# Optimization experiments

Measured on AMD Instinct MI355X. Metric: run time of the kernel, lower is better.

Reference implementation:

```python
import jax, jax.numpy as jnp
import numpy as np

EPS = 1e-3  # tfa LayerNormLSTMCell default norm epsilon

def _ln(z, g, b):
    # layernorm over last axis, per gate: z [B,4,U], g/b [4,U]
    mu = jnp.mean(z, axis=-1, keepdims=True)
    var = jnp.mean((z - mu) ** 2, axis=-1, keepdims=True)
    return g * (z - mu) * jax.lax.rsqrt(var + EPS) + b

def setup_inputs() -> dict:
    key = jax.random.key(0)
    ks = jax.random.split(key, 12)
    B, T, D, U, C = 1024, 100, 300, 512, 14
    sc = lambda k, shape, fan: jax.random.normal(k, shape, jnp.float32) * (1.0 / np.sqrt(fan))
    return {
        "x": jax.random.normal(ks[0], (B, T, D), jnp.float32),
        "mask": jax.random.randint(ks[1], (B, T), 0, 2).astype(jnp.int32),
        # layer 0 (input dim D)
        "W0": sc(ks[2], (D, 4 * U), D), "U0": sc(ks[3], (U, 4 * U), U),
        "b0": jnp.zeros((4 * U,), jnp.float32),
        "g0": jnp.ones((4, U), jnp.float32), "be0": jnp.zeros((4, U), jnp.float32),
        # layer 1 (input dim U)
        "W1": sc(ks[4], (U, 4 * U), U), "U1": sc(ks[5], (U, 4 * U), U),
        "b1": jnp.zeros((4 * U,), jnp.float32),
        "g1": jnp.ones((4, U), jnp.float32), "be1": jnp.zeros((4, U), jnp.float32),
        # dense softmax head
        "Wd": sc(ks[6], (U, C), U), "bd": jnp.zeros((C,), jnp.float32),
    }

def reference(x, mask, W0, U0, b0, g0, be0, W1, U1, b1, g1, be1, Wd, bd):
    B, T, D = x.shape
    U = W0.shape[1] // 4
    params = [(W0, U0, b0, g0, be0), (W1, U1, b1, g1, be1)]

    def step(carry, tins):
        hs, cs = carry
        xt, mt = tins                      # xt [B,D_in], mt [B]
        m = (mt > 0)[:, None]
        inp = xt
        new_hs, new_cs = [], []
        for l in range(2):
            W, Uw, b, g, be = params[l]
            z = (inp @ W + hs[l] @ Uw).reshape(B, 4, U)
            z = _ln(z, g, be) + b.reshape(4, U)
            i_g = jax.nn.sigmoid(z[:, 0])
            f_g = jax.nn.sigmoid(z[:, 1])
            c_g = jnp.tanh(z[:, 2])
            o_g = jax.nn.sigmoid(z[:, 3])
            c = f_g * cs[l] + i_g * c_g
            h = o_g * jnp.tanh(c)
            # keras RNN masking: carry state through masked steps
            h = jnp.where(m, h, hs[l])
            c = jnp.where(m, c, cs[l])
            new_hs.append(h); new_cs.append(c)
            inp = h
        return (tuple(new_hs), tuple(new_cs)), None

    z0 = jnp.zeros((B, U), x.dtype)
    carry0 = ((z0, z0), (z0, z0))
    xs = (jnp.swapaxes(x, 0, 1), mask.T)   # time-major [T,B,...]
    (hs, _), _ = jax.lax.scan(step, carry0, xs)
    h_top = hs[-1]                          # [B,U] = last valid output via mask carry
    return jax.nn.softmax(h_top @ Wd + bd, axis=-1)
```

## Files before the change

### kernel.cpp

```cpp
#include <hip/hip_runtime.h>


typedef _Float16 f16;
typedef _Float16 f16x8 __attribute__((ext_vector_type(8)));
typedef float f32x4 __attribute__((ext_vector_type(4)));

__global__ __launch_bounds__(256) void transpose_f16(
    const float* __restrict__ W, f16* __restrict__ Bt, int K, int N, int Kp,
    int k_off) {
  __shared__ float s[32][33];
  int n0 = blockIdx.x * 32, k0 = blockIdx.y * 32;
  int tid = threadIdx.x, c = tid & 31, r8 = tid >> 5;
  for (int rr = r8; rr < 32; rr += 8) {
    int k = k0 + rr;
    s[rr][c] = (k < K) ? W[(long)k * N + (n0 + c)] : 0.0f;
  }
  __syncthreads();
  for (int rr = r8; rr < 32; rr += 8)
    Bt[(long)(n0 + rr) * Kp + k_off + (k0 + c)] = (f16)s[c][rr];
}

#define MFMAS(AF, BF)                                                                   \
  acc[0][0] = __builtin_amdgcn_mfma_f32_16x16x32_f16(AF[0], BF[0], acc[0][0], 0, 0, 0); \
  acc[0][1] = __builtin_amdgcn_mfma_f32_16x16x32_f16(AF[0], BF[1], acc[0][1], 0, 0, 0); \
  acc[1][0] = __builtin_amdgcn_mfma_f32_16x16x32_f16(AF[1], BF[0], acc[1][0], 0, 0, 0); \
  acc[1][1] = __builtin_amdgcn_mfma_f32_16x16x32_f16(AF[1], BF[1], acc[1][1], 0, 0, 0); \
  acc[2][0] = __builtin_amdgcn_mfma_f32_16x16x32_f16(AF[2], BF[0], acc[2][0], 0, 0, 0); \
  acc[2][1] = __builtin_amdgcn_mfma_f32_16x16x32_f16(AF[2], BF[1], acc[2][1], 0, 0, 0); \
  acc[3][0] = __builtin_amdgcn_mfma_f32_16x16x32_f16(AF[3], BF[0], acc[3][0], 0, 0, 0); \
  acc[3][1] = __builtin_amdgcn_mfma_f32_16x16x32_f16(AF[3], BF[1], acc[3][1], 0, 0, 0);

#define LOADAB(AF, BF, A0, B0, LDB, K0)                    \
  AF[0] = *(const f16x8*)((A0) + (K0));                    \
  AF[1] = *(const f16x8*)((A0) + 16 * 1024 + (K0));        \
  AF[2] = *(const f16x8*)((A0) + 32 * 1024 + (K0));        \
  AF[3] = *(const f16x8*)((A0) + 48 * 1024 + (K0));        \
  BF[0] = *(const f16x8*)((B0) + (K0));                    \
  BF[1] = *(const f16x8*)((B0) + 16 * (LDB) + (K0));

#define GEMM_PIPE4(A0, B0, LDB, KTOT)                            \
  {                                                              \
    f16x8 aA[4], bA[2], aB[4], bB[2];                            \
    f16x8 aC[4], bC[2], aD[4], bD[2];                            \
    LOADAB(aA, bA, A0, B0, LDB, 0)                               \
    LOADAB(aB, bB, A0, B0, LDB, 32)                              \
    LOADAB(aC, bC, A0, B0, LDB, 64)                              \
    LOADAB(aD, bD, A0, B0, LDB, 96)                              \
    for (int k0 = 0; k0 + 224 < (KTOT); k0 += 128) {             \
      MFMAS(aA, bA) LOADAB(aA, bA, A0, B0, LDB, k0 + 128)        \
      MFMAS(aB, bB) LOADAB(aB, bB, A0, B0, LDB, k0 + 160)        \
      MFMAS(aC, bC) LOADAB(aC, bC, A0, B0, LDB, k0 + 192)       \
      MFMAS(aD, bD) LOADAB(aD, bD, A0, B0, LDB, k0 + 224)        \
    }                                                            \
    MFMAS(aA, bA) MFMAS(aB, bB) MFMAS(aC, bC) MFMAS(aD, bD)      \
  }

#define LOADX(AF, BF, K0)                                            \
  {                                                                  \
    _Pragma("unroll") for (int i = 0; i < 4; ++i) {                  \
      f32x4 lo = *(const f32x4*)(ax + (long)i * 4800 + (K0));        \
      f32x4 hi = *(const f32x4*)(ax + (long)i * 4800 + (K0) + 4);    \
      _Pragma("unroll") for (int e = 0; e < 4; ++e) {                \
        AF[i][e] = (f16)lo[e];                                       \
        AF[i][4 + e] = (f16)hi[e];                                   \
      }                                                              \
    }                                                                \
    BF[0] = *(const f16x8*)(bw + (K0));                              \
    BF[1] = *(const f16x8*)(bw + 16 * 320 + (K0));                   \
  }

__global__ __launch_bounds__(256) void gemm_x0(
    const float* __restrict__ x, const f16* __restrict__ W0t,
    f16* __restrict__ z0x) {
  __shared__ f16 st[64][136];
  int tid = threadIdx.x;
  int lane = tid & 63, w = tid >> 6;
  int l15 = lane & 15, quad = lane >> 4;
  long bn0 = (long)blockIdx.x * 128 + w * 32;
  long bm0 = (long)blockIdx.y * 64;
  const float* ax = x + (bm0 + l15) * 300L + quad * 8;
  const f16* bw = W0t + (bn0 + l15) * 320L + quad * 8;

  f32x4 acc[4][2] = {};
  f16x8 af0[4], bf0[2], af1[4], bf1[2];
  LOADX(af0, bf0, 0)
  for (int k0 = 0; k0 < 224; k0 += 64) {
    LOADX(af1, bf1, k0 + 32)
    MFMAS(af0, bf0)
    LOADX(af0, bf0, k0 + 64)
    MFMAS(af1, bf1)
  }
  {
#pragma unroll
    for (int i = 0; i < 4; ++i) {
      long rb = (bm0 + l15 + i * 16) * 300L;
#pragma unroll
      for (int e = 0; e < 8; ++e) {
        int k = 288 + quad * 8 + e;
        af1[i][e] = (k < 300) ? (f16)x[rb + k] : (f16)0.f;
      }
    }
    bf1[0] = *(const f16x8*)(bw + 288);
    bf1[1] = *(const f16x8*)(bw + 16 * 320 + 288);
  }
  MFMAS(af0, bf0)
  MFMAS(af1, bf1)

#pragma unroll
  for (int i = 0; i < 4; ++i)
#pragma unroll
    for (int j = 0; j < 2; ++j)
#pragma unroll
      for (int r = 0; r < 4; ++r)
        st[i * 16 + quad * 4 + r][w * 32 + j * 16 + l15] = (f16)acc[i][j][r];
  __syncthreads();

  {
    int r = tid >> 2, cc = (tid & 3) * 32;
    unsigned rr = (unsigned)(bm0 + r);
    unsigned b = rr / 100u, t = rr - b * 100u;
    f16* dst = z0x + (long)t * 2097152 + (long)b * 2048 + (long)blockIdx.x * 128 + cc;
    const f16x8* s8 = (const f16x8*)&st[r][cc];
    f16x8* d8 = (f16x8*)dst;
    d8[0] = s8[0]; d8[1] = s8[1]; d8[2] = s8[2]; d8[3] = s8[3];
  }
}

__global__ __launch_bounds__(256, 2) void gemm_step(
    const float* __restrict__ xt, const f16* __restrict__ h01,
    const f16* __restrict__ W0t, const f16* __restrict__ U0t,
    const f16* __restrict__ WU1t, const f16* __restrict__ cin0,
    float* __restrict__ zA, float* __restrict__ zB, int do0, int do1) {
  int prob = blockIdx.y >> 4;
  if (prob ? !do1 : !do0) return;
  int tid = threadIdx.x;
  int lane = tid & 63, w = tid >> 6;
  int l15 = lane & 15, quad = lane >> 4;
  long bn0 = (long)blockIdx.x * 128 + w * 32;
  long bm0 = (long)(blockIdx.y & 15) * 64;
  long arow = (bm0 + l15) * 1024 + quad * 8;

  f32x4 acc[4][2] = {};

  if (prob == 0) {
    if (!cin0) {
      const float* ax = xt + (bm0 + l15) * 30000L + quad * 8;
      const f16* bw = W0t + (bn0 + l15) * 320L + quad * 8;
#pragma unroll
      for (int k0 = 0; k0 < 288; k0 += 32) {
        f16x8 af[4], bf[2];
#pragma unroll
        for (int i = 0; i < 4; ++i) {
          f32x4 lo = *(const f32x4*)(ax + (long)i * 480000 + k0);
          f32x4 hi = *(const f32x4*)(ax + (long)i * 480000 + k0 + 4);
#pragma unroll
          for (int e = 0; e < 4; ++e) {
            af[i][e] = (f16)lo[e];
            af[i][4 + e] = (f16)hi[e];
          }
        }
        bf[0] = *(const f16x8*)(bw + k0);
        bf[1] = *(const f16x8*)(bw + 16 * 320 + k0);
        MFMAS(af, bf)
      }
      {
        f16x8 af[4], bf[2];
#pragma unroll
        for (int i = 0; i < 4; ++i) {
          long rb = (bm0 + l15 + i * 16) * 30000L;
#pragma unroll
          for (int e = 0; e < 8; ++e) {
            int k = 288 + quad * 8 + e;
            af[i][e] = (k < 300) ? (f16)xt[rb + k] : (f16)0.f;
          }
        }
        bf[0] = *(const f16x8*)(bw + 288);
        bf[1] = *(const f16x8*)(bw + 16 * 320 + 288);
        MFMAS(af, bf)
      }
    }
    {
      const f16* a0 = h01 + arow;
      const f16* b0 = U0t + (bn0 + l15) * 512L + quad * 8;
      GEMM_PIPE4(a0, b0, 512, 512)
    }
  } else {
    const f16* a0 = h01 + arow;
    const f16* b0 = WU1t + (bn0 + l15) * 1024L + quad * 8;
    GEMM_PIPE4(a0, b0, 1024, 1024)
  }

  float* Z = prob ? zB : zA;
#pragma unroll
  for (int i = 0; i < 4; ++i) {
    long row = bm0 + i * 16 + quad * 4;
#pragma unroll
    for (int j = 0; j < 2; ++j) {
      long col = bn0 + j * 16 + l15;
#pragma unroll
      for (int r = 0; r < 4; ++r) {
        float v = acc[i][j][r];
        if (prob == 0 && cin0) v += (float)cin0[(row + r) * 2048 + col];
        Z[(row + r) * 2048 + col] = v;
      }
    }
  }
}

__global__ __launch_bounds__(256) void ln_gates2(
    const float* __restrict__ zA, const float* __restrict__ zB,
    const float* __restrict__ g0, const float* __restrict__ be0,
    const float* __restrict__ b0, const float* __restrict__ g1,
    const float* __restrict__ be1, const float* __restrict__ b1,
    const int* __restrict__ mask, int t,
    f16* __restrict__ h01, float* __restrict__ c0, float* __restrict__ c1,
    int do0, int do1) {
  __shared__ float act[2048];
  int layer = blockIdx.x >> 10;
  if (layer ? !do1 : !do0) return;
  int b = blockIdx.x & 1023;
  const float* z = layer ? zB : zA;
  const float* gamma = layer ? g1 : g0;
  const float* beta = layer ? be1 : be0;
  const float* bias = layer ? b1 : b0;
  f16* h = h01 + layer * 512;
  float* c = layer ? c1 : c0;
  int tm = layer ? (t - 1) : t;

  int tid = threadIdx.x;
  int w = tid >> 6, lane = tid & 63;

  const float* zb = z + (long)b * 2048 + w * 512;
  f32x4 zv[2];
  float sum = 0.0f, sq = 0.0f;
#pragma unroll
  for (int i = 0; i < 2; ++i) {
    f32x4 v = *(const f32x4*)(zb + lane * 4 + 256 * i);
    zv[i] = v;
#pragma unroll
    for (int e = 0; e < 4; ++e) {
      sum += v[e];
      sq += v[e] * v[e];
    }
  }
#pragma unroll
  for (int off = 32; off; off >>= 1) {
    sum += __shfl_xor(sum, off);
    sq += __shfl_xor(sq, off);
  }
  float mu = sum * (1.0f / 512.0f);
  float var = sq * (1.0f / 512.0f) - mu * mu;
  float is = rsqrtf(var + 1e-3f);

#pragma unroll
  for (int i = 0; i < 2; ++i) {
    int k = w * 512 + lane * 4 + 256 * i;
    f32x4 g = *(const f32x4*)(gamma + k);
    f32x4 be = *(const f32x4*)(beta + k);
    f32x4 bi = *(const f32x4*)(bias + k);
    f32x4 av;
#pragma unroll
    for (int e = 0; e < 4; ++e) {
      float val = g[e] * (zv[i][e] - mu) * is + be[e] + bi[e];
      float a;
      if (w == 2) {
        a = 2.0f / (1.0f + __expf(-2.0f * val)) - 1.0f;
      } else {
        a = 1.0f / (1.0f + __expf(-val));
      }
      av[e] = a;
    }
    *(f32x4*)(act + k) = av;
  }
  __syncthreads();

  bool m = mask[(long)b * 100 + tm] > 0;
#pragma unroll
  for (int i = 0; i < 2; ++i) {
    int u = tid + 256 * i;
    float co = c[(long)b * 512 + u];
    float ho = (float)h[(long)b * 1024 + u];
    float cn = act[512 + u] * co + act[u] * act[1024 + u];
    float th = 2.0f / (1.0f + __expf(-2.0f * cn)) - 1.0f;
    float hn = act[1536 + u] * th;
    h[(long)b * 1024 + u] = (f16)(m ? hn : ho);
    c[(long)b * 512 + u] = m ? cn : co;
  }
}

__global__ __launch_bounds__(64) void head_kernel(
    const f16* __restrict__ h01, const float* __restrict__ Wd,
    const float* __restrict__ bd, float* __restrict__ out) {
  __shared__ float hs[512];
  __shared__ float lg[16];
  int b = blockIdx.x, tid = threadIdx.x;
#pragma unroll
  for (int i = 0; i < 8; ++i)
    hs[tid + 64 * i] = (float)h01[(long)b * 1024 + 512 + tid + 64 * i];
  __syncthreads();
  if (tid < 14) {
    float s = bd[tid];
    for (int k = 0; k < 512; ++k) s += hs[k] * Wd[k * 14 + tid];
    lg[tid] = s;
  }
  __syncthreads();
  if (tid < 14) {
    float mx = lg[0];
#pragma unroll
    for (int i = 1; i < 14; ++i) mx = fmaxf(mx, lg[i]);
    float e = __expf(lg[tid] - mx);
    float den = 0.0f;
#pragma unroll
    for (int i = 0; i < 14; ++i) den += __expf(lg[i] - mx);
    out[(long)b * 14 + tid] = e / den;
  }
}

extern "C" void kernel_launch(void* const* d_in, const int* in_sizes, int n_in,
                              void* d_out, int out_size, void* d_ws, size_t ws_size,
                              hipStream_t stream) {
  const float* x   = (const float*)d_in[0];
  const int* mask  = (const int*)d_in[1];
  const float* W0  = (const float*)d_in[2];
  const float* U0w = (const float*)d_in[3];
  const float* b0  = (const float*)d_in[4];
  const float* g0  = (const float*)d_in[5];
  const float* be0 = (const float*)d_in[6];
  const float* W1  = (const float*)d_in[7];
  const float* U1w = (const float*)d_in[8];
  const float* b1  = (const float*)d_in[9];
  const float* g1  = (const float*)d_in[10];
  const float* be1 = (const float*)d_in[11];
  const float* Wd  = (const float*)d_in[12];
  const float* bd  = (const float*)d_in[13];
  float* out = (float*)d_out;

  char* p = (char*)d_ws;
  const size_t MB = (size_t)1 << 20;
  f16*   h01  = (f16*)(p + 0);
  float* c0   = (float*)(p + 2 * MB);
  float* c1   = (float*)(p + 4 * MB);
  float* zA   = (float*)(p + 6 * MB);
  float* zB   = (float*)(p + 14 * MB);
  f16*   W0t  = (f16*)(p + 22 * MB);
  f16*   U0t  = (f16*)(p + 22 * MB + 1310720);
  f16*   WU1t = (f16*)(p + 22 * MB + 1310720 + 2097152);
  f16*   z0x  = (f16*)(p + 32 * MB);

  const bool hoist = ws_size >= (size_t)432 * MB;

  hipMemsetAsync(p, 0, 6 * MB, stream);

  transpose_f16<<<dim3(64, 10), 256, 0, stream>>>(W0,  W0t, 300, 2048, 320, 0);
  transpose_f16<<<dim3(64, 16), 256, 0, stream>>>(U0w, U0t, 512, 2048, 512, 0);
  transpose_f16<<<dim3(64, 16), 256, 0, stream>>>(W1,  WU1t, 512, 2048, 1024, 0);
  transpose_f16<<<dim3(64, 16), 256, 0, stream>>>(U1w, WU1t, 512, 2048, 1024, 512);

  if (hoist) {
    gemm_x0<<<dim3(16, 1600), 256, 0, stream>>>(x, W0t, z0x);
  }

  for (int t = 0; t <= 100; ++t) {
    int do0 = (t < 100) ? 1 : 0;
    int do1 = (t >= 1) ? 1 : 0;
    const f16* cin0 = hoist ? (z0x + (long)t * 2097152) : nullptr;
    gemm_step<<<dim3(16, 32), 256, 0, stream>>>(
        x + (long)t * 300, h01, W0t, U0t, WU1t, cin0, zA, zB, do0, do1);
    ln_gates2<<<2048, 256, 0, stream>>>(
        zA, zB, g0, be0, b0, g1, be1, b1, mask, t, h01, c0, c1, do0, do1);
  }

  head_kernel<<<1024, 64, 0, stream>>>(h01, Wd, bd, out);
}
```

Before: 5.923 ms.

## Store gate pre-activations in fp16 and stage x tile once in LDS for hoisted GEMM

```diff
diff --git a/kernel.cpp b/kernel.cpp
--- a/kernel.cpp
+++ b/kernel.cpp
@@ -3,6 +3,7 @@
 
 typedef _Float16 f16;
 typedef _Float16 f16x8 __attribute__((ext_vector_type(8)));
+typedef _Float16 f16x4 __attribute__((ext_vector_type(4)));
 typedef float f32x4 __attribute__((ext_vector_type(4)));
 
 __global__ __launch_bounds__(256) void transpose_f16(
@@ -55,74 +56,62 @@
     MFMAS(aA, bA) MFMAS(aB, bB) MFMAS(aC, bC) MFMAS(aD, bD)      \
   }
 
-#define LOADX(AF, BF, K0)                                            \
-  {                                                                  \
-    _Pragma("unroll") for (int i = 0; i < 4; ++i) {                  \
-      f32x4 lo = *(const f32x4*)(ax + (long)i * 4800 + (K0));        \
-      f32x4 hi = *(const f32x4*)(ax + (long)i * 4800 + (K0) + 4);    \
-      _Pragma("unroll") for (int e = 0; e < 4; ++e) {                \
-        AF[i][e] = (f16)lo[e];                                       \
-        AF[i][4 + e] = (f16)hi[e];                                   \
-      }                                                              \
-    }                                                                \
-    BF[0] = *(const f16x8*)(bw + (K0));                              \
-    BF[1] = *(const f16x8*)(bw + 16 * 320 + (K0));                   \
-  }
-
 __global__ __launch_bounds__(256) void gemm_x0(
     const float* __restrict__ x, const f16* __restrict__ W0t,
     f16* __restrict__ z0x) {
+  __shared__ f16 xs[64][328];
   __shared__ f16 st[64][136];
   int tid = threadIdx.x;
+  long bm0 = (long)blockIdx.x * 64;
+
+  for (int p = 0; p < 20; ++p) {
+    unsigned idx = (unsigned)tid + p * 256u;
+    unsigned r = idx / 80u, s = idx - r * 80u;
+    f16x4 h4 = {};
+    if (s < 75u) {
+      f32x4 v = *(const f32x4*)(x + (bm0 + r) * 300L + s * 4u);
+      h4[0] = (f16)v[0]; h4[1] = (f16)v[1];
+      h4[2] = (f16)v[2]; h4[3] = (f16)v[3];
+    }
+    *(f16x4*)&xs[r][s * 4u] = h4;
+  }
+  __syncthreads();
+
   int lane = tid & 63, w = tid >> 6;
   int l15 = lane & 15, quad = lane >> 4;
-  long bn0 = (long)blockIdx.x * 128 + w * 32;
-  long bm0 = (long)blockIdx.y * 64;
-  const float* ax = x + (bm0 + l15) * 300L + quad * 8;
-  const f16* bw = W0t + (bn0 + l15) * 320L + quad * 8;
-
-  f32x4 acc[4][2] = {};
-  f16x8 af0[4], bf0[2], af1[4], bf1[2];
-  LOADX(af0, bf0, 0)
-  for (int k0 = 0; k0 < 224; k0 += 64) {
-    LOADX(af1, bf1, k0 + 32)
-    MFMAS(af0, bf0)
-    LOADX(af0, bf0, k0 + 64)
-    MFMAS(af1, bf1)
-  }
-  {
-#pragma unroll
-    for (int i = 0; i < 4; ++i) {
-      long rb = (bm0 + l15 + i * 16) * 300L;
-#pragma unroll
-      for (int e = 0; e < 8; ++e) {
-        int k = 288 + quad * 8 + e;
-        af1[i][e] = (k < 300) ? (f16)x[rb + k] : (f16)0.f;
-      }
-    }
-    bf1[0] = *(const f16x8*)(bw + 288);
-    bf1[1] = *(const f16x8*)(bw + 16 * 320 + 288);
-  }
-  MFMAS(af0, bf0)
-  MFMAS(af1, bf1)
-
-#pragma unroll
-  for (int i = 0; i < 4; ++i)
-#pragma unroll
-    for (int j = 0; j < 2; ++j)
-#pragma unroll
-      for (int r = 0; r < 4; ++r)
-        st[i * 16 + quad * 4 + r][w * 32 + j * 16 + l15] = (f16)acc[i][j][r];
-  __syncthreads();
-
-  {
-    int r = tid >> 2, cc = (tid & 3) * 32;
-    unsigned rr = (unsigned)(bm0 + r);
-    unsigned b = rr / 100u, t = rr - b * 100u;
-    f16* dst = z0x + (long)t * 2097152 + (long)b * 2048 + (long)blockIdx.x * 128 + cc;
-    const f16x8* s8 = (const f16x8*)&st[r][cc];
-    f16x8* d8 = (f16x8*)dst;
-    d8[0] = s8[0]; d8[1] = s8[1]; d8[2] = s8[2]; d8[3] = s8[3];
+
+  for (int nc = 0; nc < 16; ++nc) {
+    long bn0 = (long)nc * 128 + w * 32;
+    const f16* bw = W0t + (bn0 + l15) * 320L + quad * 8;
+    f32x4 acc[4][2] = {};
+#pragma unroll
+    for (int k0 = 0; k0 < 320; k0 += 32) {
+      f16x8 af[4], bf[2];
+#pragma unroll
+      for (int i = 0; i < 4; ++i)
+        af[i] = *(const f16x8*)&xs[l15 + i * 16][quad * 8 + k0];
+      bf[0] = *(const f16x8*)(bw + k0);
+      bf[1] = *(const f16x8*)(bw + 16 * 320 + k0);
+      MFMAS(af, bf)
+    }
+    __syncthreads();
+#pragma unroll
+    for (int i = 0; i < 4; ++i)
+#pragma unroll
+      for (int j = 0; j < 2; ++j)
+#pragma unroll
+        for (int r = 0; r < 4; ++r)
+          st[i * 16 + quad * 4 + r][w * 32 + j * 16 + l15] = (f16)acc[i][j][r];
+    __syncthreads();
+    {
+      int r = tid >> 2, cc = (tid & 3) * 32;
+      unsigned rr = (unsigned)(bm0 + r);
+      unsigned b = rr / 100u, t = rr - b * 100u;
+      f16* dst = z0x + (long)t * 2097152 + (long)b * 2048 + nc * 128 + cc;
+      const f16x8* s8 = (const f16x8*)&st[r][cc];
+      f16x8* d8 = (f16x8*)dst;
+      d8[0] = s8[0]; d8[1] = s8[1]; d8[2] = s8[2]; d8[3] = s8[3];
+    }
   }
 }
 
@@ -130,7 +119,8 @@
     const float* __restrict__ xt, const f16* __restrict__ h01,
     const f16* __restrict__ W0t, const f16* __restrict__ U0t,
     const f16* __restrict__ WU1t, const f16* __restrict__ cin0,
-    float* __restrict__ zA, float* __restrict__ zB, int do0, int do1) {
+    f16* __restrict__ zA, f16* __restrict__ zB, int do0, int do1) {
+  __shared__ f16 st[64][136];
   int prob = blockIdx.y >> 4;
   if (prob ? !do1 : !do0) return;
   int tid = threadIdx.x;
@@ -190,25 +180,35 @@
     GEMM_PIPE4(a0, b0, 1024, 1024)
   }
 
-  float* Z = prob ? zB : zA;
 #pragma unroll
   for (int i = 0; i < 4; ++i) {
-    long row = bm0 + i * 16 + quad * 4;
 #pragma unroll
     for (int j = 0; j < 2; ++j) {
-      long col = bn0 + j * 16 + l15;
 #pragma unroll
       for (int r = 0; r < 4; ++r) {
         float v = acc[i][j][r];
-        if (prob == 0 && cin0) v += (float)cin0[(row + r) * 2048 + col];
-        Z[(row + r) * 2048 + col] = v;
+        if (prob == 0 && cin0) {
+          long row = bm0 + i * 16 + quad * 4 + r;
+          long col = bn0 + j * 16 + l15;
+          v += (float)cin0[row * 2048 + col];
+        }
+        st[i * 16 + quad * 4 + r][w * 32 + j * 16 + l15] = (f16)v;
       }
     }
   }
+  __syncthreads();
+  {
+    f16* Z = prob ? zB : zA;
+    int r = tid >> 2, cc = (tid & 3) * 32;
+    f16* dst = Z + (bm0 + r) * 2048 + (long)blockIdx.x * 128 + cc;
+    const f16x8* s8 = (const f16x8*)&st[r][cc];
+    f16x8* d8 = (f16x8*)dst;
+    d8[0] = s8[0]; d8[1] = s8[1]; d8[2] = s8[2]; d8[3] = s8[3];
+  }
 }
 
 __global__ __launch_bounds__(256) void ln_gates2(
-    const float* __restrict__ zA, const float* __restrict__ zB,
+    const f16* __restrict__ zA, const f16* __restrict__ zB,
     const float* __restrict__ g0, const float* __restrict__ be0,
     const float* __restrict__ b0, const float* __restrict__ g1,
     const float* __restrict__ be1, const float* __restrict__ b1,
@@ -219,7 +219,7 @@
   int layer = blockIdx.x >> 10;
   if (layer ? !do1 : !do0) return;
   int b = blockIdx.x & 1023;
-  const float* z = layer ? zB : zA;
+  const f16* z = layer ? zB : zA;
   const float* gamma = layer ? g1 : g0;
   const float* beta = layer ? be1 : be0;
   const float* bias = layer ? b1 : b0;
@@ -230,18 +230,15 @@
   int tid = threadIdx.x;
   int w = tid >> 6, lane = tid & 63;
 
-  const float* zb = z + (long)b * 2048 + w * 512;
-  f32x4 zv[2];
+  f16x8 v8 = *(const f16x8*)(z + (long)b * 2048 + w * 512 + lane * 8);
+  float zv[8];
   float sum = 0.0f, sq = 0.0f;
 #pragma unroll
-  for (int i = 0; i < 2; ++i) {
-    f32x4 v = *(const f32x4*)(zb + lane * 4 + 256 * i);
-    zv[i] = v;
-#pragma unroll
-    for (int e = 0; e < 4; ++e) {
-      sum += v[e];
-      sq += v[e] * v[e];
-    }
+  for (int e = 0; e < 8; ++e) {
+    float v = (float)v8[e];
+    zv[e] = v;
+    sum += v;
+    sq += v * v;
   }
 #pragma unroll
   for (int off = 32; off; off >>= 1) {
@@ -252,16 +249,16 @@
   float var = sq * (1.0f / 512.0f) - mu * mu;
   float is = rsqrtf(var + 1e-3f);
 
+  int k = w * 512 + lane * 8;
 #pragma unroll
   for (int i = 0; i < 2; ++i) {
-    int k = w * 512 + lane * 4 + 256 * i;
-    f32x4 g = *(const f32x4*)(gamma + k);
-    f32x4 be = *(const f32x4*)(beta + k);
-    f32x4 bi = *(const f32x4*)(bias + k);
+    f32x4 g = *(const f32x4*)(gamma + k + 4 * i);
+    f32x4 be = *(const f32x4*)(beta + k + 4 * i);
+    f32x4 bi = *(const f32x4*)(bias + k + 4 * i);
     f32x4 av;
 #pragma unroll
     for (int e = 0; e < 4; ++e) {
-      float val = g[e] * (zv[i][e] - mu) * is + be[e] + bi[e];
+      float val = g[e] * (zv[4 * i + e] - mu) * is + be[e] + bi[e];
       float a;
       if (w == 2) {
         a = 2.0f / (1.0f + __expf(-2.0f * val)) - 1.0f;
@@ -270,7 +267,7 @@
       }
       av[e] = a;
     }
-    *(f32x4*)(act + k) = av;
+    *(f32x4*)(act + k + 4 * i) = av;
   }
   __syncthreads();
 
@@ -340,11 +337,11 @@
   f16*   h01  = (f16*)(p + 0);
   float* c0   = (float*)(p + 2 * MB);
   float* c1   = (float*)(p + 4 * MB);
-  float* zA   = (float*)(p + 6 * MB);
-  float* zB   = (float*)(p + 14 * MB);
-  f16*   W0t  = (f16*)(p + 22 * MB);
-  f16*   U0t  = (f16*)(p + 22 * MB + 1310720);
-  f16*   WU1t = (f16*)(p + 22 * MB + 1310720 + 2097152);
+  f16*   zA   = (f16*)(p + 6 * MB);
+  f16*   zB   = (f16*)(p + 10 * MB);
+  f16*   W0t  = (f16*)(p + 14 * MB);
+  f16*   U0t  = (f16*)(p + 14 * MB + 1310720);
+  f16*   WU1t = (f16*)(p + 14 * MB + 1310720 + 2097152);
   f16*   z0x  = (f16*)(p + 32 * MB);
 
   const bool hoist = ws_size >= (size_t)432 * MB;
@@ -357,7 +354,7 @@
   transpose_f16<<<dim3(64, 16), 256, 0, stream>>>(U1w, WU1t, 512, 2048, 1024, 512);
 
   if (hoist) {
-    gemm_x0<<<dim3(16, 1600), 256, 0, stream>>>(x, W0t, z0x);
+    gemm_x0<<<1600, 256, 0, stream>>>(x, W0t, z0x);
   }
 
   for (int t = 0; t <= 100; ++t) {
```

Result: no change. 6.006 ms (+1.4%).

## Enlarge per-step GEMM tiles and stage input tile in LDS for x-projection

Applied to the files above, without the earlier changes.

```diff
diff --git a/kernel.cpp b/kernel.cpp
--- a/kernel.cpp
+++ b/kernel.cpp
@@ -3,6 +3,7 @@
 
 typedef _Float16 f16;
 typedef _Float16 f16x8 __attribute__((ext_vector_type(8)));
+typedef _Float16 f16x4 __attribute__((ext_vector_type(4)));
 typedef float f32x4 __attribute__((ext_vector_type(4)));
 
 __global__ __launch_bounds__(256) void transpose_f16(
@@ -30,164 +31,130 @@
   acc[3][0] = __builtin_amdgcn_mfma_f32_16x16x32_f16(AF[3], BF[0], acc[3][0], 0, 0, 0); \
   acc[3][1] = __builtin_amdgcn_mfma_f32_16x16x32_f16(AF[3], BF[1], acc[3][1], 0, 0, 0);
 
-#define LOADAB(AF, BF, A0, B0, LDB, K0)                    \
+__global__ __launch_bounds__(256) void gemm_x0(
+    const float* __restrict__ x, long lda, const f16* __restrict__ W0t,
+    f16* __restrict__ z0x, int full) {
+  __shared__ f16 xs[64][340];
+  __shared__ f16 st[64][136];
+  int tid = threadIdx.x;
+  long bm0 = (long)blockIdx.x * 64;
+
+  for (int p = 0; p < 20; ++p) {
+    unsigned idx = (unsigned)tid + p * 256u;
+    unsigned r = idx / 80u, s = idx - r * 80u;
+    f16x4 h4 = {};
+    if (s < 75u) {
+      f32x4 v = *(const f32x4*)(x + (bm0 + r) * lda + s * 4u);
+      h4[0] = (f16)v[0]; h4[1] = (f16)v[1];
+      h4[2] = (f16)v[2]; h4[3] = (f16)v[3];
+    }
+    *(f16x4*)&xs[r][s * 4u] = h4;
+  }
+  __syncthreads();
+
+  int lane = tid & 63, w = tid >> 6;
+  int l15 = lane & 15, quad = lane >> 4;
+
+  for (int nc = 0; nc < 16; ++nc) {
+    long bn0 = (long)nc * 128 + w * 32;
+    const f16* bw = W0t + (bn0 + l15) * 320L + quad * 8;
+    f32x4 acc[4][2] = {};
+#pragma unroll
+    for (int k0 = 0; k0 < 320; k0 += 32) {
+      f16x8 af[4], bf[2];
+#pragma unroll
+      for (int i = 0; i < 4; ++i)
+        af[i] = *(const f16x8*)&xs[l15 + i * 16][quad * 8 + k0];
+      bf[0] = *(const f16x8*)(bw + k0);
+      bf[1] = *(const f16x8*)(bw + 16 * 320 + k0);
+      MFMAS(af, bf)
+    }
+    __syncthreads();
+#pragma unroll
+    for (int i = 0; i < 4; ++i)
+#pragma unroll
+      for (int j = 0; j < 2; ++j)
+#pragma unroll
+        for (int r = 0; r < 4; ++r)
+          st[i * 16 + quad * 4 + r][w * 32 + j * 16 + l15] = (f16)acc[i][j][r];
+    __syncthreads();
+    {
+      int r = tid >> 2, cc = (tid & 3) * 32;
+      f16* dst;
+      if (full) {
+        unsigned rr = (unsigned)(bm0 + r);
+        unsigned b = rr / 100u, t = rr - b * 100u;
+        dst = z0x + (long)t * 2097152 + (long)b * 2048 + nc * 128 + cc;
+      } else {
+        dst = z0x + (bm0 + r) * 2048 + nc * 128 + cc;
+      }
+      const f16x8* s8 = (const f16x8*)&st[r][cc];
+      f16x8* d8 = (f16x8*)dst;
+      d8[0] = s8[0]; d8[1] = s8[1]; d8[2] = s8[2]; d8[3] = s8[3];
+    }
+  }
+}
+
+#define LD8(AF, BF, A0, B0, LDB, K0)                       \
   AF[0] = *(const f16x8*)((A0) + (K0));                    \
   AF[1] = *(const f16x8*)((A0) + 16 * 1024 + (K0));        \
   AF[2] = *(const f16x8*)((A0) + 32 * 1024 + (K0));        \
   AF[3] = *(const f16x8*)((A0) + 48 * 1024 + (K0));        \
   BF[0] = *(const f16x8*)((B0) + (K0));                    \
-  BF[1] = *(const f16x8*)((B0) + 16 * (LDB) + (K0));
-
-#define GEMM_PIPE4(A0, B0, LDB, KTOT)                            \
+  BF[1] = *(const f16x8*)((B0) + 16 * (LDB) + (K0));       \
+  BF[2] = *(const f16x8*)((B0) + 32 * (LDB) + (K0));       \
+  BF[3] = *(const f16x8*)((B0) + 48 * (LDB) + (K0));
+
+#define MM16(AF, BF)                                                              \
+  {                                                                               \
+    _Pragma("unroll") for (int i_ = 0; i_ < 4; ++i_)                              \
+    _Pragma("unroll") for (int j_ = 0; j_ < 4; ++j_)                              \
+      acc[i_][j_] = __builtin_amdgcn_mfma_f32_16x16x32_f16(AF[i_], BF[j_],        \
+                                                            acc[i_][j_], 0, 0, 0); \
+  }
+
+#define GEMM_PIPE4W(A0, B0, LDB, KTOT)                           \
   {                                                              \
-    f16x8 aA[4], bA[2], aB[4], bB[2];                            \
-    f16x8 aC[4], bC[2], aD[4], bD[2];                            \
-    LOADAB(aA, bA, A0, B0, LDB, 0)                               \
-    LOADAB(aB, bB, A0, B0, LDB, 32)                              \
-    LOADAB(aC, bC, A0, B0, LDB, 64)                              \
-    LOADAB(aD, bD, A0, B0, LDB, 96)                              \
+    f16x8 aA[4], bA[4], aB[4], bB[4];                            \
+    f16x8 aC[4], bC[4], aD[4], bD[4];                            \
+    LD8(aA, bA, A0, B0, LDB, 0)                                  \
+    LD8(aB, bB, A0, B0, LDB, 32)                                 \
+    LD8(aC, bC, A0, B0, LDB, 64)                                 \
+    LD8(aD, bD, A0, B0, LDB, 96)                                 \
     for (int k0 = 0; k0 + 224 < (KTOT); k0 += 128) {             \
-      MFMAS(aA, bA) LOADAB(aA, bA, A0, B0, LDB, k0 + 128)        \
-      MFMAS(aB, bB) LOADAB(aB, bB, A0, B0, LDB, k0 + 160)        \
-      MFMAS(aC, bC) LOADAB(aC, bC, A0, B0, LDB, k0 + 192)       \
-      MFMAS(aD, bD) LOADAB(aD, bD, A0, B0, LDB, k0 + 224)        \
+      MM16(aA, bA) LD8(aA, bA, A0, B0, LDB, k0 + 128)            \
+      MM16(aB, bB) LD8(aB, bB, A0, B0, LDB, k0 + 160)            \
+      MM16(aC, bC) LD8(aC, bC, A0, B0, LDB, k0 + 192)            \
+      MM16(aD, bD) LD8(aD, bD, A0, B0, LDB, k0 + 224)            \
     }                                                            \
-    MFMAS(aA, bA) MFMAS(aB, bB) MFMAS(aC, bC) MFMAS(aD, bD)      \
-  }
-
-#define LOADX(AF, BF, K0)                                            \
-  {                                                                  \
-    _Pragma("unroll") for (int i = 0; i < 4; ++i) {                  \
-      f32x4 lo = *(const f32x4*)(ax + (long)i * 4800 + (K0));        \
-      f32x4 hi = *(const f32x4*)(ax + (long)i * 4800 + (K0) + 4);    \
-      _Pragma("unroll") for (int e = 0; e < 4; ++e) {                \
-        AF[i][e] = (f16)lo[e];                                       \
-        AF[i][4 + e] = (f16)hi[e];                                   \
-      }                                                              \
-    }                                                                \
-    BF[0] = *(const f16x8*)(bw + (K0));                              \
-    BF[1] = *(const f16x8*)(bw + 16 * 320 + (K0));                   \
-  }
-
-__global__ __launch_bounds__(256) void gemm_x0(
-    const float* __restrict__ x, const f16* __restrict__ W0t,
-    f16* __restrict__ z0x) {
-  __shared__ f16 st[64][136];
-  int tid = threadIdx.x;
-  int lane = tid & 63, w = tid >> 6;
-  int l15 = lane & 15, quad = lane >> 4;
-  long bn0 = (long)blockIdx.x * 128 + w * 32;
-  long bm0 = (long)blockIdx.y * 64;
-  const float* ax = x + (bm0 + l15) * 300L + quad * 8;
-  const f16* bw = W0t + (bn0 + l15) * 320L + quad * 8;
-
-  f32x4 acc[4][2] = {};
-  f16x8 af0[4], bf0[2], af1[4], bf1[2];
-  LOADX(af0, bf0, 0)
-  for (int k0 = 0; k0 < 224; k0 += 64) {
-    LOADX(af1, bf1, k0 + 32)
-    MFMAS(af0, bf0)
-    LOADX(af0, bf0, k0 + 64)
-    MFMAS(af1, bf1)
-  }
-  {
-#pragma unroll
-    for (int i = 0; i < 4; ++i) {
-      long rb = (bm0 + l15 + i * 16) * 300L;
-#pragma unroll
-      for (int e = 0; e < 8; ++e) {
-        int k = 288 + quad * 8 + e;
-        af1[i][e] = (k < 300) ? (f16)x[rb + k] : (f16)0.f;
-      }
-    }
-    bf1[0] = *(const f16x8*)(bw + 288);
-    bf1[1] = *(const f16x8*)(bw + 16 * 320 + 288);
-  }
-  MFMAS(af0, bf0)
-  MFMAS(af1, bf1)
-
-#pragma unroll
-  for (int i = 0; i < 4; ++i)
-#pragma unroll
-    for (int j = 0; j < 2; ++j)
-#pragma unroll
-      for (int r = 0; r < 4; ++r)
-        st[i * 16 + quad * 4 + r][w * 32 + j * 16 + l15] = (f16)acc[i][j][r];
-  __syncthreads();
-
-  {
-    int r = tid >> 2, cc = (tid & 3) * 32;
-    unsigned rr = (unsigned)(bm0 + r);
-    unsigned b = rr / 100u, t = rr - b * 100u;
-    f16* dst = z0x + (long)t * 2097152 + (long)b * 2048 + (long)blockIdx.x * 128 + cc;
-    const f16x8* s8 = (const f16x8*)&st[r][cc];
-    f16x8* d8 = (f16x8*)dst;
-    d8[0] = s8[0]; d8[1] = s8[1]; d8[2] = s8[2]; d8[3] = s8[3];
-  }
-}
-
-__global__ __launch_bounds__(256, 2) void gemm_step(
-    const float* __restrict__ xt, const f16* __restrict__ h01,
-    const f16* __restrict__ W0t, const f16* __restrict__ U0t,
+    MM16(aA, bA) MM16(aB, bB) MM16(aC, bC) MM16(aD, bD)          \
+  }
+
+__global__ __launch_bounds__(256, 1) void gemm_step(
+    const f16* __restrict__ h01, const f16* __restrict__ U0t,
     const f16* __restrict__ WU1t, const f16* __restrict__ cin0,
     float* __restrict__ zA, float* __restrict__ zB, int do0, int do1) {
-  int prob = blockIdx.y >> 4;
+  int y = blockIdx.y;
+  int prob = y >> 3;
   if (prob ? !do1 : !do0) return;
   int tid = threadIdx.x;
   int lane = tid & 63, w = tid >> 6;
+  int wr = w >> 1, wc = w & 1;
   int l15 = lane & 15, quad = lane >> 4;
-  long bn0 = (long)blockIdx.x * 128 + w * 32;
-  long bm0 = (long)(blockIdx.y & 15) * 64;
+  long bm0 = (long)(y & 7) * 128 + wr * 64;
+  long bn0 = (long)blockIdx.x * 128 + wc * 64;
   long arow = (bm0 + l15) * 1024 + quad * 8;
 
-  f32x4 acc[4][2] = {};
+  f32x4 acc[4][4] = {};
 
   if (prob == 0) {
-    if (!cin0) {
-      const float* ax = xt + (bm0 + l15) * 30000L + quad * 8;
-      const f16* bw = W0t + (bn0 + l15) * 320L + quad * 8;
-#pragma unroll
-      for (int k0 = 0; k0 < 288; k0 += 32) {
-        f16x8 af[4], bf[2];
-#pragma unroll
-        for (int i = 0; i < 4; ++i) {
-          f32x4 lo = *(const f32x4*)(ax + (long)i * 480000 + k0);
-          f32x4 hi = *(const f32x4*)(ax + (long)i * 480000 + k0 + 4);
-#pragma unroll
-          for (int e = 0; e < 4; ++e) {
-            af[i][e] = (f16)lo[e];
-            af[i][4 + e] = (f16)hi[e];
-          }
-        }
-        bf[0] = *(const f16x8*)(bw + k0);
-        bf[1] = *(const f16x8*)(bw + 16 * 320 + k0);
-        MFMAS(af, bf)
-      }
-      {
-        f16x8 af[4], bf[2];
-#pragma unroll
-        for (int i = 0; i < 4; ++i) {
-          long rb = (bm0 + l15 + i * 16) * 30000L;
-#pragma unroll
-          for (int e = 0; e < 8; ++e) {
-            int k = 288 + quad * 8 + e;
-            af[i][e] = (k < 300) ? (f16)xt[rb + k] : (f16)0.f;
-          }
-        }
-        bf[0] = *(const f16x8*)(bw + 288);
-        bf[1] = *(const f16x8*)(bw + 16 * 320 + 288);
-        MFMAS(af, bf)
-      }
-    }
-    {
-      const f16* a0 = h01 + arow;
-      const f16* b0 = U0t + (bn0 + l15) * 512L + quad * 8;
-      GEMM_PIPE4(a0, b0, 512, 512)
-    }
+    const f16* a0 = h01 + arow;
+    const f16* b0 = U0t + (bn0 + l15) * 512L + quad * 8;
+    GEMM_PIPE4W(a0, b0, 512, 512)
   } else {
     const f16* a0 = h01 + arow;
     const f16* b0 = WU1t + (bn0 + l15) * 1024L + quad * 8;
-    GEMM_PIPE4(a0, b0, 1024, 1024)
+    GEMM_PIPE4W(a0, b0, 1024, 1024)
   }
 
   float* Z = prob ? zB : zA;
@@ -195,12 +162,12 @@
   for (int i = 0; i < 4; ++i) {
     long row = bm0 + i * 16 + quad * 4;
 #pragma unroll
-    for (int j = 0; j < 2; ++j) {
+    for (int j = 0; j < 4; ++j) {
       long col = bn0 + j * 16 + l15;
 #pragma unroll
       for (int r = 0; r < 4; ++r) {
         float v = acc[i][j][r];
-        if (prob == 0 && cin0) v += (float)cin0[(row + r) * 2048 + col];
+        if (prob == 0) v += (float)cin0[(row + r) * 2048 + col];
         Z[(row + r) * 2048 + col] = v;
       }
     }
@@ -210,8 +177,8 @@
 __global__ __launch_bounds__(256) void ln_gates2(
     const float* __restrict__ zA, const float* __restrict__ zB,
     const float* __restrict__ g0, const float* __restrict__ be0,
-    const float* __restrict__ b0, const float* __restrict__ g1,
-    const float* __restrict__ be1, const float* __restrict__ b1,
+    const float* __restrict__ bs0, const float* __restrict__ g1,
+    const float* __restrict__ be1, const float* __restrict__ bs1,
     const int* __restrict__ mask, int t,
     f16* __restrict__ h01, float* __restrict__ c0, float* __restrict__ c1,
     int do0, int do1) {
@@ -222,7 +189,7 @@
   const float* z = layer ? zB : zA;
   const float* gamma = layer ? g1 : g0;
   const float* beta = layer ? be1 : be0;
-  const float* bias = layer ? b1 : b0;
+  const float* bias = layer ? bs1 : bs0;
   f16* h = h01 + layer * 512;
   float* c = layer ? c1 : c0;
   int tm = layer ? (t - 1) : t;
@@ -345,9 +312,10 @@
   f16*   W0t  = (f16*)(p + 22 * MB);
   f16*   U0t  = (f16*)(p + 22 * MB + 1310720);
   f16*   WU1t = (f16*)(p + 22 * MB + 1310720 + 2097152);
-  f16*   z0x  = (f16*)(p + 32 * MB);
-
-  const bool hoist = ws_size >= (size_t)432 * MB;
+  f16*   zX   = (f16*)(p + 30 * MB);
+  f16*   z0x  = (f16*)(p + 34 * MB);
+
+  const bool hoist = ws_size >= (size_t)434 * MB;
 
   hipMemsetAsync(p, 0, 6 * MB, stream);
 
@@ -357,15 +325,21 @@
   transpose_f16<<<dim3(64, 16), 256, 0, stream>>>(U1w, WU1t, 512, 2048, 1024, 512);
 
   if (hoist) {
-    gemm_x0<<<dim3(16, 1600), 256, 0, stream>>>(x, W0t, z0x);
+    gemm_x0<<<1600, 256, 0, stream>>>(x, 300, W0t, z0x, 1);
   }
 
   for (int t = 0; t <= 100; ++t) {
     int do0 = (t < 100) ? 1 : 0;
     int do1 = (t >= 1) ? 1 : 0;
-    const f16* cin0 = hoist ? (z0x + (long)t * 2097152) : nullptr;
-    gemm_step<<<dim3(16, 32), 256, 0, stream>>>(
-        x + (long)t * 300, h01, W0t, U0t, WU1t, cin0, zA, zB, do0, do1);
+    const f16* cin0;
+    if (hoist) {
+      cin0 = z0x + (long)t * 2097152;
+    } else {
+      if (do0) gemm_x0<<<16, 256, 0, stream>>>(x + (long)t * 300, 30000, W0t, zX, 0);
+      cin0 = zX;
+    }
+    gemm_step<<<dim3(16, 16), 256, 0, stream>>>(
+        h01, U0t, WU1t, cin0, zA, zB, do0, do1);
     ln_gates2<<<2048, 256, 0, stream>>>(
         zA, zB, g0, be0, b0, g1, be1, b1, mask, t, h01, c0, c1, do0, do1);
   }
```

Result: faster. 5.156 ms (-13.0%).
